# Kernel optimization log

Measured on AMD Instinct MI355X. Metric: run time of the kernel, lower is better.

The kernel has to match this reference:

```python
import jax, jax.numpy as jnp
import numpy as np

B = 2          # batch_size
F = 686364     # num_node_features (full grid)
N = 65536      # num ocean nodes per sample (sum of nan_mask)
E = 1048576    # total batched edges (~degree 8)
H = 256        # embed_dim
OUT = 256      # out_features
DEPTH = 8      # extra GCNConv layers beyond conv1


def setup_inputs() -> dict:
    key = jax.random.key(0)
    ks = jax.random.split(key, 8)
    sst = jax.random.normal(ks[0], (B, F), jnp.float32)
    mask_idx = jnp.sort(jax.random.randint(ks[1], (N,), 0, F))
    edge_index = jax.random.randint(ks[2], (2, E), 0, B * N)
    # GCNConv weights stored as [in, out] (PyG stores [out, in] and does x @ W.T; same math)
    W1 = jax.random.normal(ks[3], (1, H), jnp.float32) * 0.1
    b1 = jnp.zeros((H,), jnp.float32)
    Ws = jax.random.normal(ks[4], (DEPTH, H, H), jnp.float32) * (1.0 / np.sqrt(H))
    bs = jnp.zeros((DEPTH, H), jnp.float32)
    # NOTE: original zero-inits the head (FiLM trick); random init used to avoid degenerate all-zero output
    Wh = jax.random.normal(ks[5], (H, OUT), jnp.float32) * 0.02
    bh = jax.random.normal(ks[6], (OUT,), jnp.float32) * 0.02
    return dict(sst=sst, mask_idx=mask_idx, edge_index=edge_index,
                W1=W1, b1=b1, Ws=Ws, bs=bs, Wh=Wh, bh=bh)


def reference(sst, mask_idx, edge_index, W1, b1, Ws, bs, Wh, bh):
    Bv = sst.shape[0]
    Nv = mask_idx.shape[0]
    NT = Bv * Nv
    # x = sst[batch_nan_mask][None].T  ->  [NT, 1]
    x = sst[:, mask_idx].reshape(NT, 1)
    src, dst = edge_index[0], edge_index[1]
    # gcn_norm with self-loops (cached=True: computed once, shared by all layers)
    deg = jax.ops.segment_sum(jnp.ones((src.shape[0],), sst.dtype), dst,
                              num_segments=NT) + 1.0  # +1 for self-loop
    dis = jax.lax.rsqrt(deg)                  # deg^{-1/2}
    norm = (dis[src] * dis[dst])[:, None]     # [E, 1]
    self_norm = (dis * dis)[:, None]          # self-loop weight = 1/deg

    def conv(h, W, b):
        hw = h @ W                                             # linear transform
        agg = jax.ops.segment_sum(norm * hw[src], dst,         # gather -> scale -> scatter-add
                                  num_segments=NT)
        agg = agg + self_norm * hw                             # self-loop contribution
        return agg + b

    x = x + jax.nn.leaky_relu(conv(x, W1, b1))   # [NT,1] broadcasts to [NT,H]
    for i in range(Ws.shape[0]):
        x = x + jax.nn.leaky_relu(conv(x, Ws[i], bs[i]))
    # global_mean_pool with batch = arange(B) repeated per node == contiguous segment mean
    pooled = x.reshape(Bv, Nv, -1).mean(axis=1)  # [B, H]
    return pooled @ Wh + bh                      # head_film
```

## Files before the change

### kernel.cpp

```cpp
#include <hip/hip_runtime.h>

typedef unsigned short ushort_t;
typedef _Float16 f16x8 __attribute__((ext_vector_type(8)));
typedef float f32x4 __attribute__((ext_vector_type(4)));
typedef float f32x2 __attribute__((ext_vector_type(2)));
typedef unsigned short us8 __attribute__((ext_vector_type(8)));

#define H_DIM 256
#define OUT_DIM 256

__device__ inline float lrelu(float v) { return v > 0.f ? v : 0.01f * v; }

__device__ inline unsigned short f2h(float f) {
    _Float16 h = (_Float16)f;
    unsigned short u;
    __builtin_memcpy(&u, &h, 2);
    return u;
}

__device__ inline float h2f(unsigned short u) {
    _Float16 h;
    __builtin_memcpy(&h, &u, 2);
    return (float)h;
}


__global__ void k_gather_x0(const float* __restrict__ sst, const int* __restrict__ mask,
                            float* __restrict__ x0, int NT, int Nn, int F) {
    int v = blockIdx.x * 256 + threadIdx.x;
    if (v < NT) {
        int b = v / Nn;
        int i = v - b * Nn;
        x0[v] = sst[(size_t)b * F + mask[i]];
    }
}

__global__ void k_count(const int* __restrict__ dst, int* __restrict__ cnt,
                        int* __restrict__ rank, int E) {
    int e = blockIdx.x * 256 + threadIdx.x;
    if (e < E) rank[e] = atomicAdd(&cnt[dst[e]], 1);
}

__global__ void k_dis(const int* __restrict__ cnt, float* __restrict__ dis, int NT) {
    int v = blockIdx.x * 256 + threadIdx.x;
    if (v < NT) dis[v] = rsqrtf((float)cnt[v] + 1.0f);
}

__global__ void k_scan_block(const int* __restrict__ cnt, int* __restrict__ bsum, int NT) {
    __shared__ int s[256];
    int i = blockIdx.x * 256 + threadIdx.x;
    s[threadIdx.x] = (i < NT) ? cnt[i] : 0;
    __syncthreads();
    for (int o = 128; o > 0; o >>= 1) {
        if (threadIdx.x < o) s[threadIdx.x] += s[threadIdx.x + o];
        __syncthreads();
    }
    if (threadIdx.x == 0) bsum[blockIdx.x] = s[0];
}

__global__ void k_scan_top(const int* __restrict__ bsum, int* __restrict__ bpre, int nb) {
    __shared__ int s[512];
    int t = threadIdx.x;
    int v = (t < nb) ? bsum[t] : 0;
    s[t] = v;
    __syncthreads();
    for (int o = 1; o < nb; o <<= 1) {
        int add = (t >= o) ? s[t - o] : 0;
        __syncthreads();
        s[t] += add;
        __syncthreads();
    }
    if (t < nb) bpre[t] = s[t] - v;
}

__global__ void k_scan_scatter(const int* __restrict__ cnt, const int* __restrict__ bpre,
                               int* __restrict__ startp, int NT) {
    __shared__ int s[256];
    int t = threadIdx.x;
    int i = blockIdx.x * 256 + t;
    int v = (i < NT) ? cnt[i] : 0;
    s[t] = v;
    __syncthreads();
    for (int o = 1; o < 256; o <<= 1) {
        int add = (t >= o) ? s[t - o] : 0;
        __syncthreads();
        s[t] += add;
        __syncthreads();
    }
    int excl = s[t] - v + bpre[blockIdx.x];
    if (i < NT) startp[i] = excl;
}

__global__ void k_fill(const int* __restrict__ src, const int* __restrict__ dst,
                       const int* __restrict__ rank, const int* __restrict__ startp,
                       const float* __restrict__ dis, int2* __restrict__ ecsr, int E) {
    int e = blockIdx.x * 256 + threadIdx.x;
    if (e < E) {
        int s = src[e], d = dst[e];
        float nw = dis[s] * dis[d];
        int p = startp[d] + rank[e];
        ecsr[p] = make_int2(s, __float_as_int(nw));
    }
}

__global__ void k_prepW(const float* __restrict__ Ws, ushort_t* __restrict__ Wt, int total) {
    int idx = blockIdx.x * 256 + threadIdx.x;
    if (idx < total) {
        int l = idx >> 16;
        int rem = idx & 65535;
        int k = rem >> 8;
        int n = rem & 255;
        Wt[(l << 16) + (n << 8) + k] = f2h(Ws[idx]);
    }
}


__global__ void k_agg0(const float* __restrict__ x0, const int* __restrict__ startp,
                       const int* __restrict__ cnt, const int2* __restrict__ ecsr,
                       const float* __restrict__ dis, float* __restrict__ y0, int NT) {
    int v = blockIdx.x * 256 + threadIdx.x;
    if (v >= NT) return;
    float d = dis[v];
    float acc = d * d * x0[v];
    int s = startp[v], e = s + cnt[v];
    for (int i = s; i < e; i++) {
        int2 ec = ecsr[i];
        acc += __int_as_float(ec.y) * x0[ec.x];
    }
    y0[v] = acc;
}

__global__ void k_expand(const float* __restrict__ x0, const float* __restrict__ y0,
                         const float* __restrict__ W1, const float* __restrict__ b1,
                         ushort_t* __restrict__ xh, int NT) {
    int idx = blockIdx.x * 256 + threadIdx.x;
    int v = idx >> 6;
    int q = idx & 63;
    if (v >= NT) return;
    float xv = x0[v], yv = y0[v];
    float4 w = ((const float4*)W1)[q];
    float4 b = ((const float4*)b1)[q];
    ushort4 o;
    o.x = f2h(xv + lrelu(yv * w.x + b.x));
    o.y = f2h(xv + lrelu(yv * w.y + b.y));
    o.z = f2h(xv + lrelu(yv * w.z + b.z));
    o.w = f2h(xv + lrelu(yv * w.w + b.w));
    ((ushort4*)xh)[(size_t)v * 64 + q] = o;
}


__global__ __launch_bounds__(256) void k_gemm(const ushort_t* __restrict__ xh,
                                              const ushort_t* __restrict__ Wt,
                                              unsigned char* __restrict__ z, int NT) {
    __shared__ __align__(16) char AsRaw[64 * 512];
    __shared__ __align__(16) char Rep[4][4096];
    int tid = threadIdx.x;
    int wave = tid >> 6, lane = tid & 63;
    int rl = lane & 15, hi = lane >> 4;

    f16x8 bf[4][8];
    #pragma unroll
    for (int ni = 0; ni < 4; ni++)
        #pragma unroll
        for (int c = 0; c < 8; c++)
            bf[ni][c] = *(const f16x8*)(Wt + (size_t)(wave * 64 + ni * 16 + rl) * 256
                                        + c * 32 + hi * 8);

    int ntiles = NT / 64;
    for (int t = blockIdx.x; t < ntiles; t += gridDim.x) {
        size_t rowbase = (size_t)t * 64;

        #pragma unroll
        for (int p = 0; p < 8; p++) {
            int idx = p * 256 + tid;
            int row = idx >> 5;
            int colb = (idx & 31) * 16;
            uint4 vsrc = *(const uint4*)(xh + (rowbase + row) * H_DIM + (idx & 31) * 8);
            *(uint4*)(AsRaw + row * 512 + (colb ^ ((row & 7) << 4))) = vsrc;
        }
        __syncthreads();

        f32x4 acc[4][4];
        #pragma unroll
        for (int mi = 0; mi < 4; mi++)
            #pragma unroll
            for (int ni = 0; ni < 4; ni++)
                acc[mi][ni] = (f32x4){0.f, 0.f, 0.f, 0.f};

        #pragma unroll
        for (int c = 0; c < 8; c++) {
            f16x8 af[4];
            #pragma unroll
            for (int mi = 0; mi < 4; mi++) {
                int row = mi * 16 + rl;
                int colb = c * 64 + hi * 16;
                af[mi] = *(const f16x8*)(AsRaw + row * 512 + (colb ^ ((row & 7) << 4)));
            }
            #pragma unroll
            for (int mi = 0; mi < 4; mi++)
                #pragma unroll
                for (int ni = 0; ni < 4; ni++)
                    acc[mi][ni] = __builtin_amdgcn_mfma_f32_16x16x32_f16(
                        af[mi], bf[ni][c], acc[mi][ni], 0, 0, 0);
        }
        __syncthreads();

        char* slice = &Rep[wave][0];
        #pragma unroll
        for (int mi = 0; mi < 4; mi++)
            #pragma unroll
            for (int ni = 0; ni < 4; ni++)
                #pragma unroll
                for (int r = 0; r < 4; r++) {
                    float vv = acc[mi][ni][r];
                    int pk = __builtin_amdgcn_cvt_pk_fp8_f32(vv, vv, 0, false);
                    slice[(mi * 16 + hi * 4 + r) * 64 + ni * 16 + rl] = (char)(pk & 0xFF);
                }
        #pragma unroll
        for (int p = 0; p < 4; p++) {
            uint4 val = *(const uint4*)(slice + p * 1024 + lane * 16);
            int lrow = p * 16 + (lane >> 2);
            int lcolb = (lane & 3) * 16;
            *(uint4*)(z + (rowbase + lrow) * 256 + wave * 64 + lcolb) = val;
        }
    }
}


__global__ void k_aggres(const unsigned char* __restrict__ z, const int* __restrict__ startp,
                         const int* __restrict__ cnt, const int2* __restrict__ ecsr,
                         const float* __restrict__ dis, const float* __restrict__ bias,
                         ushort_t* __restrict__ xh, int NT) {
    int tid = threadIdx.x;
    int wave = tid >> 6, lane = tid & 63;
    int h = lane >> 5, hl = lane & 31;
    int v = blockIdx.x * 8 + wave * 2 + h;
    if (v >= NT) return;

    float d = dis[v];
    int s = startp[v], cv = cnt[v];

    int nsrc = 0;
    float nw = 0.f;
    if (hl < cv) {
        int2 ec = ecsr[s + hl];
        nsrc = ec.x;
        nw = __int_as_float(ec.y);
    }

    int cv0 = __shfl(cv, 0);
    int cv1 = __shfl(cv, 32);
    int cvmax = cv0 > cv1 ? cv0 : cv1;
    int inl = cvmax > 32 ? 32 : cvmax;
    int iters = (inl + 3) & ~3;

    uint2 a = *(const uint2*)(z + (size_t)v * 256 + hl * 8);
    us8 xr = *(const us8*)(xh + (size_t)v * H_DIM + hl * 8);
    float4 bv0 = *(const float4*)(bias + hl * 8);
    float4 bv1 = *(const float4*)(bias + hl * 8 + 4);

    float sn = d * d;
    float acc[8];
    {
        f32x2 p0 = __builtin_amdgcn_cvt_pk_f32_fp8(a.x, false);
        f32x2 p1 = __builtin_amdgcn_cvt_pk_f32_fp8(a.x, true);
        f32x2 p2 = __builtin_amdgcn_cvt_pk_f32_fp8(a.y, false);
        f32x2 p3 = __builtin_amdgcn_cvt_pk_f32_fp8(a.y, true);
        acc[0] = sn * p0[0]; acc[1] = sn * p0[1];
        acc[2] = sn * p1[0]; acc[3] = sn * p1[1];
        acc[4] = sn * p2[0]; acc[5] = sn * p2[1];
        acc[6] = sn * p3[0]; acc[7] = sn * p3[1];
    }

    int base = h << 5;
    for (int k = 0; k < iters; k += 4) {
        int i0 = __shfl(nsrc, base + k);     float w0 = __shfl(nw, base + k);
        int i1 = __shfl(nsrc, base + k + 1); float w1 = __shfl(nw, base + k + 1);
        int i2 = __shfl(nsrc, base + k + 2); float w2 = __shfl(nw, base + k + 2);
        int i3 = __shfl(nsrc, base + k + 3); float w3 = __shfl(nw, base + k + 3);
        uint2 b0 = *(const uint2*)(z + (size_t)i0 * 256 + hl * 8);
        uint2 b1 = *(const uint2*)(z + (size_t)i1 * 256 + hl * 8);
        uint2 b2 = *(const uint2*)(z + (size_t)i2 * 256 + hl * 8);
        uint2 b3 = *(const uint2*)(z + (size_t)i3 * 256 + hl * 8);
        #pragma unroll
        for (int e4 = 0; e4 < 4; e4++) {
            uint2 bb = e4 == 0 ? b0 : (e4 == 1 ? b1 : (e4 == 2 ? b2 : b3));
            float ww = e4 == 0 ? w0 : (e4 == 1 ? w1 : (e4 == 2 ? w2 : w3));
            f32x2 p0 = __builtin_amdgcn_cvt_pk_f32_fp8(bb.x, false);
            f32x2 p1 = __builtin_amdgcn_cvt_pk_f32_fp8(bb.x, true);
            f32x2 p2 = __builtin_amdgcn_cvt_pk_f32_fp8(bb.y, false);
            f32x2 p3 = __builtin_amdgcn_cvt_pk_f32_fp8(bb.y, true);
            acc[0] += ww * p0[0]; acc[1] += ww * p0[1];
            acc[2] += ww * p1[0]; acc[3] += ww * p1[1];
            acc[4] += ww * p2[0]; acc[5] += ww * p2[1];
            acc[6] += ww * p3[0]; acc[7] += ww * p3[1];
        }
    }
    for (int k = 32; k < cv; k++) {
        int2 ec = ecsr[s + k];
        float ww = __int_as_float(ec.y);
        uint2 bb = *(const uint2*)(z + (size_t)ec.x * 256 + hl * 8);
        f32x2 p0 = __builtin_amdgcn_cvt_pk_f32_fp8(bb.x, false);
        f32x2 p1 = __builtin_amdgcn_cvt_pk_f32_fp8(bb.x, true);
        f32x2 p2 = __builtin_amdgcn_cvt_pk_f32_fp8(bb.y, false);
        f32x2 p3 = __builtin_amdgcn_cvt_pk_f32_fp8(bb.y, true);
        acc[0] += ww * p0[0]; acc[1] += ww * p0[1];
        acc[2] += ww * p1[0]; acc[3] += ww * p1[1];
        acc[4] += ww * p2[0]; acc[5] += ww * p2[1];
        acc[6] += ww * p3[0]; acc[7] += ww * p3[1];
    }

    us8 o;
    o[0] = f2h(h2f(xr[0]) + lrelu(acc[0] + bv0.x));
    o[1] = f2h(h2f(xr[1]) + lrelu(acc[1] + bv0.y));
    o[2] = f2h(h2f(xr[2]) + lrelu(acc[2] + bv0.z));
    o[3] = f2h(h2f(xr[3]) + lrelu(acc[3] + bv0.w));
    o[4] = f2h(h2f(xr[4]) + lrelu(acc[4] + bv1.x));
    o[5] = f2h(h2f(xr[5]) + lrelu(acc[5] + bv1.y));
    o[6] = f2h(h2f(xr[6]) + lrelu(acc[6] + bv1.z));
    o[7] = f2h(h2f(xr[7]) + lrelu(acc[7] + bv1.w));
    *(us8*)(xh + (size_t)v * H_DIM + hl * 8) = o;
}


__global__ void k_pool1(const ushort_t* __restrict__ xh, float* __restrict__ partial) {
    __shared__ float s[4][256];
    int t = threadIdx.x;
    int w = t >> 6, lane = t & 63;
    size_t nodebase = (size_t)blockIdx.x * 64;
    float4 acc = make_float4(0.f, 0.f, 0.f, 0.f);
    for (int i = 0; i < 16; i++) {
        size_t node = nodebase + i * 4 + w;
        ushort4 v = *(const ushort4*)(xh + node * H_DIM + lane * 4);
        acc.x += h2f(v.x); acc.y += h2f(v.y); acc.z += h2f(v.z); acc.w += h2f(v.w);
    }
    *(float4*)&s[w][lane * 4] = acc;
    __syncthreads();
    float sum = s[0][t] + s[1][t] + s[2][t] + s[3][t];
    partial[(size_t)blockIdx.x * H_DIM + t] = sum;
}

__global__ void k_pool2(const float* __restrict__ partial, float* __restrict__ partial2,
                        int rowsPerChunk) {
    int blk = blockIdx.x, t = threadIdx.x;
    size_t rowbase = (size_t)blk * rowsPerChunk;
    float s = 0.f;
    for (int j = 0; j < rowsPerChunk; j++)
        s += partial[(rowbase + j) * H_DIM + t];
    partial2[(size_t)blk * H_DIM + t] = s;
}

__global__ void k_pool3(const float* __restrict__ partial2, float* __restrict__ pooled,
                        int chunksPerBatch, float inv) {
    int b = blockIdx.x, t = threadIdx.x;
    float s = 0.f;
    for (int j = 0; j < chunksPerBatch; j++)
        s += partial2[((size_t)b * chunksPerBatch + j) * H_DIM + t];
    pooled[b * H_DIM + t] = s * inv;
}

__global__ void k_head(const float* __restrict__ pooled, const float* __restrict__ Wh,
                       const float* __restrict__ bh, float* __restrict__ out) {
    int b = blockIdx.x, o = threadIdx.x;
    float acc = bh[o];
    for (int h = 0; h < H_DIM; h++) acc += pooled[b * H_DIM + h] * Wh[h * OUT_DIM + o];
    out[b * OUT_DIM + o] = acc;
}


extern "C" void kernel_launch(void* const* d_in, const int* in_sizes, int n_in,
                              void* d_out, int out_size, void* d_ws, size_t ws_size,
                              hipStream_t stream) {
    const float* sst  = (const float*)d_in[0];
    const int*   mask = (const int*)d_in[1];
    const int*   eidx = (const int*)d_in[2];
    const float* W1   = (const float*)d_in[3];
    const float* b1   = (const float*)d_in[4];
    const float* Ws   = (const float*)d_in[5];
    const float* bs   = (const float*)d_in[6];
    const float* Wh   = (const float*)d_in[7];
    const float* bh   = (const float*)d_in[8];

    const int B  = out_size / OUT_DIM;
    const int Nn = in_sizes[1];
    const int E  = in_sizes[2] / 2;
    const int F  = in_sizes[0] / B;
    const int DEPTH = in_sizes[5] / (H_DIM * H_DIM);
    const int NT = B * Nn;

    size_t off = 0;
    char* base = (char*)d_ws;
    auto alloc = [&](size_t bytes) -> void* {
        void* p = base + off;
        off += (bytes + 255) & ~(size_t)255;
        return p;
    };
    ushort_t*      xh      = (ushort_t*)alloc((size_t)NT * H_DIM * 2);
    unsigned char* zbuf    = (unsigned char*)alloc((size_t)NT * 256);
    float*    x0      = (float*)alloc((size_t)NT * 4);
    float*    y0      = (float*)alloc((size_t)NT * 4);
    int*      cnt     = (int*)alloc((size_t)NT * 4);
    int*      startp  = (int*)alloc((size_t)NT * 4);
    float*    dis     = (float*)alloc((size_t)NT * 4);
    int*      bsum    = (int*)alloc(4096);
    int*      bpre    = (int*)alloc(4096);
    int*      rank    = (int*)alloc((size_t)E * 4);
    int2*     ecsr    = (int2*)alloc((size_t)E * 8);
    ushort_t* Wt      = (ushort_t*)alloc((size_t)DEPTH * H_DIM * H_DIM * 2);
    float*    partial = (float*)alloc((size_t)(NT / 64) * H_DIM * 4);
    float*    partial2= (float*)alloc((size_t)64 * H_DIM * 4);
    float*    pooled  = (float*)alloc((size_t)B * H_DIM * 4);
    if (off > ws_size) return;

    const int* esrc = eidx;
    const int* edst = eidx + E;

    dim3 blk(256);
    int gNT = (NT + 255) / 256;
    int gE  = (E + 255) / 256;
    int nb  = gNT;

    hipMemsetAsync(cnt, 0, (size_t)NT * 4, stream);

    k_gather_x0<<<gNT, blk, 0, stream>>>(sst, mask, x0, NT, Nn, F);
    k_count<<<gE, blk, 0, stream>>>(edst, cnt, rank, E);
    k_dis<<<gNT, blk, 0, stream>>>(cnt, dis, NT);
    k_scan_block<<<nb, blk, 0, stream>>>(cnt, bsum, NT);
    k_scan_top<<<1, 512, 0, stream>>>(bsum, bpre, nb);
    k_scan_scatter<<<nb, blk, 0, stream>>>(cnt, bpre, startp, NT);
    k_fill<<<gE, blk, 0, stream>>>(esrc, edst, rank, startp, dis, ecsr, E);
    k_prepW<<<(DEPTH * H_DIM * H_DIM + 255) / 256, blk, 0, stream>>>(Ws, Wt, DEPTH * H_DIM * H_DIM);

    k_agg0<<<gNT, blk, 0, stream>>>(x0, startp, cnt, ecsr, dis, y0, NT);
    k_expand<<<(NT * 64 + 255) / 256, blk, 0, stream>>>(x0, y0, W1, b1, xh, NT);

    for (int l = 0; l < DEPTH; l++) {
        k_gemm<<<512, blk, 0, stream>>>(xh, Wt + (size_t)l * H_DIM * H_DIM, zbuf, NT);
        k_aggres<<<NT / 8, blk, 0, stream>>>(zbuf, startp, cnt, ecsr, dis,
                                             bs + (size_t)l * H_DIM, xh, NT);
    }

    int pblocks = NT / 64;
    int chunksPerBatch = 16;
    int rowsPerChunk = (pblocks / B) / chunksPerBatch;
    k_pool1<<<pblocks, blk, 0, stream>>>(xh, partial);
    k_pool2<<<B * chunksPerBatch, blk, 0, stream>>>(partial, partial2, rowsPerChunk);
    k_pool3<<<B, blk, 0, stream>>>(partial2, pooled, chunksPerBatch, 1.0f / (float)Nn);
    k_head<<<B, blk, 0, stream>>>(pooled, Wh, bh, (float*)d_out);
}
```

Baseline: 849.0 us.

## Sort nodes by degree for aggregation, unroll gathers by 8, double GEMM grid

Adds a degree-bucketed node permutation (histogram, scan, fill) so each wave's two half-wave nodes have similar neighbour counts. This cuts the padded iterations lost when paired nodes differ in degree. The aggregation loop now issues eight gathers per iteration instead of four, giving more loads in flight at the cost of more padding and registers. The GEMM launch grid is doubled, which only helps if the kernel distributes work by grid size. The permutation also scatters xh/z accesses, trading some memory locality for better load balance.

```diff
diff --git a/kernel.cpp b/kernel.cpp
--- a/kernel.cpp
+++ b/kernel.cpp
@@ -100,6 +100,44 @@
         float nw = dis[s] * dis[d];
         int p = startp[d] + rank[e];
         ecsr[p] = make_int2(s, __float_as_int(nw));
+    }
+}
+
+
+__global__ void k_dhist(const int* __restrict__ cnt, int* __restrict__ dcnt,
+                        int* __restrict__ dloc, int NT) {
+    __shared__ int h[65];
+    __shared__ int basebuf[65];
+    int t = threadIdx.x;
+    if (t < 65) h[t] = 0;
+    __syncthreads();
+    int v = blockIdx.x * 256 + t;
+    int bin = 0, lr = 0;
+    if (v < NT) {
+        int c = cnt[v];
+        bin = c > 64 ? 64 : c;
+        lr = atomicAdd(&h[bin], 1);
+    }
+    __syncthreads();
+    if (t < 65) basebuf[t] = (h[t] > 0) ? atomicAdd(&dcnt[t], h[t]) : 0;
+    __syncthreads();
+    if (v < NT) dloc[v] = basebuf[bin] + lr;
+}
+
+__global__ void k_dscan(const int* __restrict__ dcnt, int* __restrict__ dstart) {
+    if (threadIdx.x == 0) {
+        int acc = 0;
+        for (int b = 0; b < 65; b++) { dstart[b] = acc; acc += dcnt[b]; }
+    }
+}
+
+__global__ void k_dfill(const int* __restrict__ cnt, const int* __restrict__ dloc,
+                        const int* __restrict__ dstart, int* __restrict__ perm, int NT) {
+    int v = blockIdx.x * 256 + threadIdx.x;
+    if (v < NT) {
+        int c = cnt[v];
+        int bin = c > 64 ? 64 : c;
+        perm[dstart[bin] + dloc[v]] = v;
     }
 }
 
@@ -229,13 +267,14 @@
 
 __global__ void k_aggres(const unsigned char* __restrict__ z, const int* __restrict__ startp,
                          const int* __restrict__ cnt, const int2* __restrict__ ecsr,
-                         const float* __restrict__ dis, const float* __restrict__ bias,
-                         ushort_t* __restrict__ xh, int NT) {
+                         const int* __restrict__ perm, const float* __restrict__ dis,
+                         const float* __restrict__ bias, ushort_t* __restrict__ xh, int NT) {
     int tid = threadIdx.x;
     int wave = tid >> 6, lane = tid & 63;
     int h = lane >> 5, hl = lane & 31;
-    int v = blockIdx.x * 8 + wave * 2 + h;
-    if (v >= NT) return;
+    int pidx = blockIdx.x * 8 + wave * 2 + h;
+    if (pidx >= NT) return;
+    int v = perm[pidx];
 
     float d = dis[v];
     int s = startp[v], cv = cnt[v];
@@ -252,7 +291,7 @@
     int cv1 = __shfl(cv, 32);
     int cvmax = cv0 > cv1 ? cv0 : cv1;
     int inl = cvmax > 32 ? 32 : cvmax;
-    int iters = (inl + 3) & ~3;
+    int iters = (inl + 7) & ~7;
 
     uint2 a = *(const uint2*)(z + (size_t)v * 256 + hl * 8);
     us8 xr = *(const us8*)(xh + (size_t)v * H_DIM + hl * 8);
@@ -273,23 +312,25 @@
     }
 
     int base = h << 5;
-    for (int k = 0; k < iters; k += 4) {
-        int i0 = __shfl(nsrc, base + k);     float w0 = __shfl(nw, base + k);
-        int i1 = __shfl(nsrc, base + k + 1); float w1 = __shfl(nw, base + k + 1);
-        int i2 = __shfl(nsrc, base + k + 2); float w2 = __shfl(nw, base + k + 2);
-        int i3 = __shfl(nsrc, base + k + 3); float w3 = __shfl(nw, base + k + 3);
-        uint2 b0 = *(const uint2*)(z + (size_t)i0 * 256 + hl * 8);
-        uint2 b1 = *(const uint2*)(z + (size_t)i1 * 256 + hl * 8);
-        uint2 b2 = *(const uint2*)(z + (size_t)i2 * 256 + hl * 8);
-        uint2 b3 = *(const uint2*)(z + (size_t)i3 * 256 + hl * 8);
-        #pragma unroll
-        for (int e4 = 0; e4 < 4; e4++) {
-            uint2 bb = e4 == 0 ? b0 : (e4 == 1 ? b1 : (e4 == 2 ? b2 : b3));
-            float ww = e4 == 0 ? w0 : (e4 == 1 ? w1 : (e4 == 2 ? w2 : w3));
-            f32x2 p0 = __builtin_amdgcn_cvt_pk_f32_fp8(bb.x, false);
-            f32x2 p1 = __builtin_amdgcn_cvt_pk_f32_fp8(bb.x, true);
-            f32x2 p2 = __builtin_amdgcn_cvt_pk_f32_fp8(bb.y, false);
-            f32x2 p3 = __builtin_amdgcn_cvt_pk_f32_fp8(bb.y, true);
+    for (int k = 0; k < iters; k += 8) {
+        int idx[8];
+        float w[8];
+        #pragma unroll
+        for (int j = 0; j < 8; j++) {
+            idx[j] = __shfl(nsrc, base + k + j);
+            w[j]   = __shfl(nw,   base + k + j);
+        }
+        uint2 b[8];
+        #pragma unroll
+        for (int j = 0; j < 8; j++)
+            b[j] = *(const uint2*)(z + (size_t)idx[j] * 256 + hl * 8);
+        #pragma unroll
+        for (int j = 0; j < 8; j++) {
+            f32x2 p0 = __builtin_amdgcn_cvt_pk_f32_fp8(b[j].x, false);
+            f32x2 p1 = __builtin_amdgcn_cvt_pk_f32_fp8(b[j].x, true);
+            f32x2 p2 = __builtin_amdgcn_cvt_pk_f32_fp8(b[j].y, false);
+            f32x2 p3 = __builtin_amdgcn_cvt_pk_f32_fp8(b[j].y, true);
+            float ww = w[j];
             acc[0] += ww * p0[0]; acc[1] += ww * p0[1];
             acc[2] += ww * p1[0]; acc[3] += ww * p1[1];
             acc[4] += ww * p2[0]; acc[5] += ww * p2[1];
@@ -406,6 +447,10 @@
     int*      bpre    = (int*)alloc(4096);
     int*      rank    = (int*)alloc((size_t)E * 4);
     int2*     ecsr    = (int2*)alloc((size_t)E * 8);
+    int*      dcnt    = (int*)alloc(4096);
+    int*      dstart  = (int*)alloc(4096);
+    int*      dloc    = (int*)alloc((size_t)NT * 4);
+    int*      perm    = (int*)alloc((size_t)NT * 4);
     ushort_t* Wt      = (ushort_t*)alloc((size_t)DEPTH * H_DIM * H_DIM * 2);
     float*    partial = (float*)alloc((size_t)(NT / 64) * H_DIM * 4);
     float*    partial2= (float*)alloc((size_t)64 * H_DIM * 4);
@@ -421,6 +466,7 @@
     int nb  = gNT;
 
     hipMemsetAsync(cnt, 0, (size_t)NT * 4, stream);
+    hipMemsetAsync(dcnt, 0, 4096, stream);
 
     k_gather_x0<<<gNT, blk, 0, stream>>>(sst, mask, x0, NT, Nn, F);
     k_count<<<gE, blk, 0, stream>>>(edst, cnt, rank, E);
@@ -429,14 +475,17 @@
     k_scan_top<<<1, 512, 0, stream>>>(bsum, bpre, nb);
     k_scan_scatter<<<nb, blk, 0, stream>>>(cnt, bpre, startp, NT);
     k_fill<<<gE, blk, 0, stream>>>(esrc, edst, rank, startp, dis, ecsr, E);
+    k_dhist<<<gNT, blk, 0, stream>>>(cnt, dcnt, dloc, NT);
+    k_dscan<<<1, 64, 0, stream>>>(dcnt, dstart);
+    k_dfill<<<gNT, blk, 0, stream>>>(cnt, dloc, dstart, perm, NT);
     k_prepW<<<(DEPTH * H_DIM * H_DIM + 255) / 256, blk, 0, stream>>>(Ws, Wt, DEPTH * H_DIM * H_DIM);
 
     k_agg0<<<gNT, blk, 0, stream>>>(x0, startp, cnt, ecsr, dis, y0, NT);
     k_expand<<<(NT * 64 + 255) / 256, blk, 0, stream>>>(x0, y0, W1, b1, xh, NT);
 
     for (int l = 0; l < DEPTH; l++) {
-        k_gemm<<<512, blk, 0, stream>>>(xh, Wt + (size_t)l * H_DIM * H_DIM, zbuf, NT);
-        k_aggres<<<NT / 8, blk, 0, stream>>>(zbuf, startp, cnt, ecsr, dis,
+        k_gemm<<<1024, blk, 0, stream>>>(xh, Wt + (size_t)l * H_DIM * H_DIM, zbuf, NT);
+        k_aggres<<<NT / 8, blk, 0, stream>>>(zbuf, startp, cnt, ecsr, perm, dis,
                                              bs + (size_t)l * H_DIM, xh, NT);
     }
 
```

New measurement: 948.7 us. +11.7%, slower.
